# Optimization experiments

Hardware: AMD Instinct MI355X
Metric: run time of the kernel (lower is better)

## Reference

```python
import jax, jax.numpy as jnp
import numpy as np

BS, SEQ, IN, H, L = 32, 2048, 512, 256, 2


def _cell(x_t, h, W1, b1, W2, b2):
    # blending1(x, x, x): gate1*x + (1-gate1)*x  (kept literal for faithfulness)
    g1 = jax.nn.sigmoid(x_t @ W1.T + b1)
    left = g1 * x_t + (1.0 - g1) * x_t
    # blending2(h, x, x): gate from x, blend h and x
    g2 = jax.nn.sigmoid(x_t @ W2.T + b2)
    right = g2 * h + (1.0 - g2) * x_t
    return jnp.tanh(left * right)


def _run_dir(x_seq, h0, W1, b1, W2, b2):
    # x_seq: [seq, bs, H]; sequential recurrence via scan
    def step(h, x_t):
        h_new = _cell(x_t, h, W1, b1, W2, b2)
        return h_new, h_new
    h_last, ys = jax.lax.scan(step, h0, x_seq)
    return ys, h_last  # ys: [seq, bs, H], h_last: [bs, H]


def setup_inputs() -> dict:
    key = jax.random.key(0)
    ks = jax.random.split(key, 7)
    std = 1.0 / np.sqrt(H)
    return {
        "x": jax.random.normal(ks[0], (BS, SEQ, IN), dtype=jnp.float32),
        "W_fc": jax.random.uniform(ks[1], (H, IN), jnp.float32, -std, std),
        "b_fc": jax.random.uniform(ks[2], (H,), jnp.float32, -std, std),
        "W1": jax.random.uniform(ks[3], (L, H, H), jnp.float32, -std, std),
        "b1": jax.random.uniform(ks[4], (L, H), jnp.float32, -std, std),
        "W2": jax.random.uniform(ks[5], (L, H, H), jnp.float32, -std, std),
        "b2": jax.random.uniform(ks[6], (L, H), jnp.float32, -std, std),
    }


def reference(x, W_fc, b_fc, W1, b1, W2, b2):
    bs, seq, _ = x.shape
    Hh = W_fc.shape[0]
    n_layers = W1.shape[0]
    # input projection, then duplicate along features: [bs, seq, 2H]
    h = x @ W_fc.T + b_fc
    xx = jnp.concatenate([h, h], axis=2)
    h_finals = []
    for i in range(n_layers):
        # split halves: left-to-right on first half, right-to-left on flipped second half
        ltr = jnp.swapaxes(xx[:, :, :Hh], 0, 1)                      # [seq, bs, H]
        rtl = jnp.swapaxes(jnp.flip(xx[:, :, Hh:], axis=1), 0, 1)    # [seq, bs, H]
        h0 = jnp.zeros((bs, Hh), dtype=xx.dtype)
        y_l, h_l = _run_dir(ltr, h0, W1[i], b1[i], W2[i], b2[i])
        y_r, h_r = _run_dir(rtl, h0, W1[i], b1[i], W2[i], b2[i])
        y_l = jnp.swapaxes(y_l, 0, 1)                                # [bs, seq, H]
        y_r = jnp.flip(jnp.swapaxes(y_r, 0, 1), axis=1)
        xx = jnp.concatenate([y_l, y_r], axis=2)                     # [bs, seq, 2H]
        h_finals.append(jnp.stack([h_l, h_r], axis=0))               # [2, bs, H]
    h_out = jnp.concatenate(h_finals, axis=0)                        # [2L, bs, H]
    return xx, h_out
```

## Files before the change

### kernel.cpp

```cpp
#include <hip/hip_runtime.h>

#define SEQL 2048
#define BSZ  32
#define HDIM 256
#define MTOT (BSZ*SEQL)
#define XXN  ((size_t)MTOT*512)

typedef short v8s __attribute__((ext_vector_type(8)));
typedef float v4f __attribute__((ext_vector_type(4)));
typedef const __attribute__((address_space(1))) void* gptr_t;
typedef __attribute__((address_space(3))) void* sptr_t;

__device__ __forceinline__ short f2bf(float f) {
  return __builtin_bit_cast(short, (__bf16)f);
}

__device__ __forceinline__ void gload16(const float* g, float* l) {
  __builtin_amdgcn_global_load_lds((gptr_t)g, (sptr_t)l, 16, 0, 0);
}

__global__ __launch_bounds__(256) void gemm_bias_act(
    const float* __restrict__ A, int sa,
    const float* __restrict__ W, int K,
    const float* __restrict__ bias,
    float* __restrict__ C, int act)
{
  __shared__ float lds[16384];

  int tid  = threadIdx.x;
  int m0   = blockIdx.x * 128;
  int n0   = blockIdx.y * 128;
  int lane = tid & 63;
  int w    = tid >> 6;
  int wr   = w >> 1, wc = w & 1;
  int quad = lane >> 4, r16 = lane & 15;

  int lrow = lane >> 3;
  int js   = (lane & 7) ^ lrow;
  const float* aSrc = A + (long)(m0 + w*8 + lrow)*sa + js*4;
  const float* wSrc = W + (long)(n0 + w*8 + lrow)*K  + js*4;
  float* ldsA = lds + w*256;
  float* ldsB = lds + 4096 + w*256;

  auto stage = [&](int buf, int kk) {
    const float* a = aSrc + kk;
    const float* b = wSrc + kk;
    float* la = ldsA + buf*8192;
    float* lb = ldsB + buf*8192;
    #pragma unroll
    for (int i = 0; i < 4; ++i) {
      gload16(a + (long)i*32*sa, la + i*1024);
      gload16(b + (long)i*32*K,  lb + i*1024);
    }
  };

  int aoff[4][2], boff[4][2];
  #pragma unroll
  for (int i = 0; i < 4; ++i) {
    int ra = wr*64 + i*16 + r16, sA = ra & 7;
    aoff[i][0] = ra*32 + ((2*quad)     ^ sA)*4;
    aoff[i][1] = ra*32 + ((2*quad + 1) ^ sA)*4;
    int rb = wc*64 + i*16 + r16, sB = rb & 7;
    boff[i][0] = rb*32 + ((2*quad)     ^ sB)*4;
    boff[i][1] = rb*32 + ((2*quad + 1) ^ sB)*4;
  }

  auto loadfrag = [&](const float* base, const int* o) {
    float4 f0 = *(const float4*)(base + o[0]);
    float4 f1 = *(const float4*)(base + o[1]);
    v8s r;
    r[0] = f2bf(f0.x); r[1] = f2bf(f0.y); r[2] = f2bf(f0.z); r[3] = f2bf(f0.w);
    r[4] = f2bf(f1.x); r[5] = f2bf(f1.y); r[6] = f2bf(f1.z); r[7] = f2bf(f1.w);
    return r;
  };

  v4f acc[4][4];
  #pragma unroll
  for (int i = 0; i < 4; ++i)
    #pragma unroll
    for (int j = 0; j < 4; ++j)
      acc[i][j] = (v4f){0.f, 0.f, 0.f, 0.f};

  stage(0, 0);
  int nt = K >> 5;
  for (int t = 0; t < nt; ++t) {
    __syncthreads();
    if (t + 1 < nt) stage((t + 1) & 1, (t + 1) * 32);
    const float* Ab = lds + (t & 1)*8192;
    const float* Bb = Ab + 4096;
    v8s af[4], bfv[4];
    #pragma unroll
    for (int i = 0; i < 4; ++i) af[i]  = loadfrag(Ab, aoff[i]);
    #pragma unroll
    for (int j = 0; j < 4; ++j) bfv[j] = loadfrag(Bb, boff[j]);
    #pragma unroll
    for (int i = 0; i < 4; ++i)
      #pragma unroll
      for (int j = 0; j < 4; ++j)
        acc[i][j] = __builtin_amdgcn_mfma_f32_16x16x32_bf16(af[i], bfv[j], acc[i][j], 0, 0, 0);
  }

  #pragma unroll
  for (int j = 0; j < 4; ++j) {
    int col = n0 + wc*64 + j*16 + r16;
    float bv = bias[col];
    #pragma unroll
    for (int i = 0; i < 4; ++i) {
      int rowb = m0 + wr*64 + i*16 + quad*4;
      #pragma unroll
      for (int r = 0; r < 4; ++r) {
        float v = acc[i][j][r] + bv;
        if (act) {
          float e = __builtin_amdgcn_exp2f(v * -1.4426950408889634f);
          v = __builtin_amdgcn_rcpf(1.f + e);
        }
        C[(long)(rowb + r)*HDIM + col] = v;
      }
    }
  }
}

__global__ __launch_bounds__(64) void recur(
    const float* __restrict__ X, int sx, int xoffR,
    const float* __restrict__ G, int sg, int goffR,
    float* __restrict__ Y, float* __restrict__ hout)
{
  const int T = 16;
  const int SEGS = 8;
  const int SEGLEN = SEQL / SEGS;
  const int WARM = 64;

  int blk = blockIdx.x & 255;
  int seg = blockIdx.x >> 8;
  int fg = blk & 3;
  int b  = (blk >> 2) & 31;
  int d  = blk >> 7;
  int f  = fg*64 + threadIdx.x;

  int u0    = seg*SEGLEN - (seg ? WARM : 0);
  int warmc = seg ? (WARM/T) : 0;
  int nc    = warmc + SEGLEN/T;
  int half  = nc >> 1;

  int stp  = d ? -1 : 1;
  int t0   = d ? (SEQL-1 - u0) : u0;
  int xoff = d ? xoffR : 0;
  int goff = d ? goffR : 0;

  const float* xc = X + (long)(b*SEQL + t0)*sx + xoff + f;
  const float* gc = G + (long)(b*SEQL + t0)*sg + goff + f;
  long xstep = (long)stp * sx;
  long gstep = (long)stp * sg;

  int ty0 = d ? (SEQL-1 - seg*SEGLEN) : seg*SEGLEN;
  float* yp = Y + (long)(b*SEQL + ty0)*512 + d*HDIM + f;
  long ystep = (long)stp * 512;

  const float K   = 2.8853900817779268f;
  const float mK2 = -5.7707801635558537f;

  float Ax[T], Ag[T], Bx[T], Bg[T], hb[T];
  #pragma unroll
  for (int j = 0; j < T; ++j) { Ax[j] = xc[xstep*j]; Ag[j] = gc[gstep*j]; }

  float r = 0.5f;

  auto compute = [&](float* xb, float* gb) {
    #pragma unroll
    for (int j = 0; j < T; ++j) {
      float x = xb[j], g = gb[j];
      float a = x * g;
      float m = a * mK2;
      float n = K * fmaf(x, x - a, a);
      float q = fmaf(m, r, n);
      float E = __builtin_amdgcn_exp2f(q);
      r = __builtin_amdgcn_rcpf(E + 1.0f);
      hb[j] = fmaf(-2.0f, r, 1.0f);
    }
  };
  auto flush = [&](int c) {
    if (c >= warmc) {
      #pragma unroll
      for (int j = 0; j < T; ++j) yp[ystep*j] = hb[j];
      yp += ystep*T;
    }
  };

  int c = 0;
  for (int it = 0; it < half; ++it) {
    const float* xn = xc + xstep*T;
    const float* gn = gc + gstep*T;
    #pragma unroll
    for (int j = 0; j < T; ++j) { Bx[j] = xn[xstep*j]; Bg[j] = gn[gstep*j]; }
    compute(Ax, Ag); flush(c);
    bool hv = (c+2 < nc);
    const float* xn2 = hv ? xn + xstep*T : xn;
    const float* gn2 = hv ? gn + gstep*T : gn;
    #pragma unroll
    for (int j = 0; j < T; ++j) { Ax[j] = xn2[xstep*j]; Ag[j] = gn2[gstep*j]; }
    compute(Bx, Bg); flush(c+1);
    xc = xn2; gc = gn2; c += 2;
  }

  if (seg == SEGS-1)
    hout[(size_t)d*BSZ*HDIM + (size_t)b*HDIM + f] = fmaf(-2.0f, r, 1.0f);
}

extern "C" void kernel_launch(void* const* d_in, const int* in_sizes, int n_in,
                              void* d_out, int out_size, void* d_ws, size_t ws_size,
                              hipStream_t stream) {
  const float* x    = (const float*)d_in[0];
  const float* W_fc = (const float*)d_in[1];
  const float* b_fc = (const float*)d_in[2];
  const float* W2   = (const float*)d_in[5];
  const float* b2   = (const float*)d_in[6];

  float* out  = (float*)d_out;
  float* bufA = (float*)d_ws;
  float* bufB = bufA + (size_t)MTOT*HDIM;
  float* xx   = out;
  float* hout = out + XXN;

  gemm_bias_act<<<dim3(512,2), 256, 0, stream>>>(x, 512, W_fc, 512, b_fc, bufA, 0);
  gemm_bias_act<<<dim3(512,2), 256, 0, stream>>>(bufA, HDIM, W2, HDIM, b2, bufB, 1);
  recur<<<2048, 64, 0, stream>>>(bufA, HDIM, 0, bufB, HDIM, 0, xx, hout);
  gemm_bias_act<<<dim3(1024,2), 256, 0, stream>>>(xx, HDIM, W2 + HDIM*HDIM, HDIM, b2 + HDIM, bufA, 1);
  recur<<<2048, 64, 0, stream>>>(xx, 512, 256, bufA, 512, 256, xx, hout + 2*BSZ*HDIM);
}
```

Measured before the change: 524.9 us.

## Triple-buffer A tiles with explicit waitcnt and remap GEMM blocks across XCDs

The GEMM now keeps three LDS buffers for the A operand and two for B. It issues loads two stages ahead and replaces __syncthreads with an explicit partial vmcnt wait plus s_barrier, so global-to-LDS loads overlap more of the MFMA work. The grid is flattened to 1D and block IDs are remapped so that consecutive tiles, which share the same A rows for both N halves, land on the same XCD and get better L2 reuse. LDS use grows from 64 KB to 80 KB per block, which may reduce occupancy, and the hand-written vmcnt counts must match the number of outstanding loads exactly.

```diff
diff --git a/kernel.cpp b/kernel.cpp
--- a/kernel.cpp
+++ b/kernel.cpp
@@ -25,11 +25,16 @@
     const float* __restrict__ bias,
     float* __restrict__ C, int act)
 {
-  __shared__ float lds[16384];
+  __shared__ float lds[20480];
 
   int tid  = threadIdx.x;
-  int m0   = blockIdx.x * 128;
-  int n0   = blockIdx.y * 128;
+  int nwg = (int)gridDim.x;
+  int cpx = nwg >> 3;
+  int bid = (int)blockIdx.x;
+  int v   = (bid & 7) * cpx + (bid >> 3);
+  int m0  = (v >> 1) * 128;
+  int n0  = (v & 1) * 128;
+
   int lane = tid & 63;
   int w    = tid >> 6;
   int wr   = w >> 1, wc = w & 1;
@@ -39,30 +44,29 @@
   int js   = (lane & 7) ^ lrow;
   const float* aSrc = A + (long)(m0 + w*8 + lrow)*sa + js*4;
   const float* wSrc = W + (long)(n0 + w*8 + lrow)*K  + js*4;
-  float* ldsA = lds + w*256;
-  float* ldsB = lds + 4096 + w*256;
-
-  auto stage = [&](int buf, int kk) {
+
+  auto stageA = [&](int buf, int kk) {
     const float* a = aSrc + kk;
+    float* la = lds + buf*4096 + w*256;
+    #pragma unroll
+    for (int i = 0; i < 4; ++i) gload16(a + (long)i*32*sa, la + i*1024);
+  };
+  auto stageB = [&](int buf, int kk) {
     const float* b = wSrc + kk;
-    float* la = ldsA + buf*8192;
-    float* lb = ldsB + buf*8192;
-    #pragma unroll
-    for (int i = 0; i < 4; ++i) {
-      gload16(a + (long)i*32*sa, la + i*1024);
-      gload16(b + (long)i*32*K,  lb + i*1024);
-    }
+    float* lb = lds + 12288 + buf*4096 + w*256;
+    #pragma unroll
+    for (int i = 0; i < 4; ++i) gload16(b + (long)i*32*K, lb + i*1024);
   };
 
   int aoff[4][2], boff[4][2];
   #pragma unroll
   for (int i = 0; i < 4; ++i) {
-    int ra = wr*64 + i*16 + r16, sA = ra & 7;
-    aoff[i][0] = ra*32 + ((2*quad)     ^ sA)*4;
-    aoff[i][1] = ra*32 + ((2*quad + 1) ^ sA)*4;
-    int rb = wc*64 + i*16 + r16, sB = rb & 7;
-    boff[i][0] = rb*32 + ((2*quad)     ^ sB)*4;
-    boff[i][1] = rb*32 + ((2*quad + 1) ^ sB)*4;
+    int ra_ = wr*64 + i*16 + r16, sA = ra_ & 7;
+    aoff[i][0] = ra_*32 + ((2*quad)     ^ sA)*4;
+    aoff[i][1] = ra_*32 + ((2*quad + 1) ^ sA)*4;
+    int rb_ = wc*64 + i*16 + r16, sB = rb_ & 7;
+    boff[i][0] = rb_*32 + ((2*quad)     ^ sB)*4;
+    boff[i][1] = rb_*32 + ((2*quad + 1) ^ sB)*4;
   }
 
   auto loadfrag = [&](const float* base, const int* o) {
@@ -81,13 +85,7 @@
     for (int j = 0; j < 4; ++j)
       acc[i][j] = (v4f){0.f, 0.f, 0.f, 0.f};
 
-  stage(0, 0);
-  int nt = K >> 5;
-  for (int t = 0; t < nt; ++t) {
-    __syncthreads();
-    if (t + 1 < nt) stage((t + 1) & 1, (t + 1) * 32);
-    const float* Ab = lds + (t & 1)*8192;
-    const float* Bb = Ab + 4096;
+  auto compute = [&](const float* Ab, const float* Bb) {
     v8s af[4], bfv[4];
     #pragma unroll
     for (int i = 0; i < 4; ++i) af[i]  = loadfrag(Ab, aoff[i]);
@@ -98,7 +96,35 @@
       #pragma unroll
       for (int j = 0; j < 4; ++j)
         acc[i][j] = __builtin_amdgcn_mfma_f32_16x16x32_bf16(af[i], bfv[j], acc[i][j], 0, 0, 0);
-  }
+  };
+
+  stageB(0, 0);
+  asm volatile("" ::: "memory");
+  stageA(0, 0);
+  asm volatile("" ::: "memory");
+  stageA(1, 32);
+
+  int nt = K >> 5;
+  int ra = 0;
+  for (int t = 0; t < nt - 1; ++t) {
+    asm volatile("s_waitcnt vmcnt(4) lgkmcnt(0)" ::: "memory");
+    __builtin_amdgcn_s_barrier();
+    asm volatile("" ::: "memory");
+
+    stageB((t + 1) & 1, (t + 1) * 32);
+    asm volatile("" ::: "memory");
+    if (t + 2 < nt) {
+      int wb = ra + 2; if (wb >= 3) wb -= 3;
+      stageA(wb, (t + 2) * 32);
+    }
+
+    compute(lds + ra*4096, lds + 12288 + (t & 1)*4096);
+    ra = (ra == 2) ? 0 : ra + 1;
+  }
+  asm volatile("s_waitcnt vmcnt(0) lgkmcnt(0)" ::: "memory");
+  __builtin_amdgcn_s_barrier();
+  asm volatile("" ::: "memory");
+  compute(lds + ra*4096, lds + 12288 + ((nt - 1) & 1)*4096);
 
   #pragma unroll
   for (int j = 0; j < 4; ++j) {
@@ -109,12 +135,12 @@
       int rowb = m0 + wr*64 + i*16 + quad*4;
       #pragma unroll
       for (int r = 0; r < 4; ++r) {
-        float v = acc[i][j][r] + bv;
+        float vv = acc[i][j][r] + bv;
         if (act) {
-          float e = __builtin_amdgcn_exp2f(v * -1.4426950408889634f);
-          v = __builtin_amdgcn_rcpf(1.f + e);
+          float e = __builtin_amdgcn_exp2f(vv * -1.4426950408889634f);
+          vv = __builtin_amdgcn_rcpf(1.f + e);
         }
-        C[(long)(rowb + r)*HDIM + col] = v;
+        C[(long)(rowb + r)*HDIM + col] = vv;
       }
     }
   }
@@ -221,9 +247,9 @@
   float* xx   = out;
   float* hout = out + XXN;
 
-  gemm_bias_act<<<dim3(512,2), 256, 0, stream>>>(x, 512, W_fc, 512, b_fc, bufA, 0);
-  gemm_bias_act<<<dim3(512,2), 256, 0, stream>>>(bufA, HDIM, W2, HDIM, b2, bufB, 1);
+  gemm_bias_act<<<1024, 256, 0, stream>>>(x, 512, W_fc, 512, b_fc, bufA, 0);
+  gemm_bias_act<<<1024, 256, 0, stream>>>(bufA, HDIM, W2, HDIM, b2, bufB, 1);
   recur<<<2048, 64, 0, stream>>>(bufA, HDIM, 0, bufB, HDIM, 0, xx, hout);
-  gemm_bias_act<<<dim3(1024,2), 256, 0, stream>>>(xx, HDIM, W2 + HDIM*HDIM, HDIM, b2 + HDIM, bufA, 1);
+  gemm_bias_act<<<2048, 256, 0, stream>>>(xx, HDIM, W2 + HDIM*HDIM, HDIM, b2 + HDIM, bufA, 1);
   recur<<<2048, 64, 0, stream>>>(xx, 512, 256, bufA, 512, 256, xx, hout + 2*BSZ*HDIM);
 }
```

New measurement: 472.4 us. 1.11x faster.
